# Kernel tuning notes

Measured on AMD Instinct MI355X. Metric: run time of the kernel, lower is better.

Reference implementation:

```python
import jax, jax.numpy as jnp
import numpy as np

B, L, HEADS, D_HEAD = 2, 2048, 16, 64
D_MODEL = HEADS * D_HEAD            # 1024
D_BI = D_MODEL * 4 // 2             # 2048 (bilinear GLU width)
D_PROJ = D_MODEL * 3 + 2 * D_BI
DEPTH = 0                           # block depth < 2 -> token shift active
NEG_INF = -1e10


def _ln(x, g, b, eps=1e-5):
    m = jnp.mean(x, axis=-1, keepdims=True)
    v = jnp.var(x, axis=-1, keepdims=True)
    return (x - m) * jax.lax.rsqrt(v + eps) * g + b


def _shift(x, n):
    # F.pad(x, (0,0,n,-n)): shift along seq dim by n, zero-fill at front
    return jnp.pad(x, ((0, 0), (n, 0), (0, 0)))[:, : x.shape[1], :]


def setup_inputs() -> dict:
    key = jax.random.key(0)
    ks = jax.random.split(key, 3)
    x = jax.random.normal(ks[0], (B, L, D_MODEL), jnp.float32)
    w_in = jax.random.normal(ks[1], (D_MODEL, D_PROJ), jnp.float32) * (D_MODEL ** -0.5)
    # note: torch init zeros out_proj; we use small random weights so backward is non-trivial
    w_out = jax.random.normal(ks[2], (D_MODEL + D_BI, D_MODEL), jnp.float32) * 0.02
    slopes = jnp.concatenate([2.0 ** jnp.linspace(0.0, -6.0, HEADS // 2),
                              jnp.zeros(HEADS - HEADS // 2)]).astype(jnp.float32)
    return {
        "x": x,
        "in_ln_g": jnp.ones(D_MODEL, jnp.float32), "in_ln_b": jnp.zeros(D_MODEL, jnp.float32),
        "mid_ln_g": jnp.ones(D_PROJ, jnp.float32), "mid_ln_b": jnp.zeros(D_PROJ, jnp.float32),
        "out_ln_g": jnp.ones(D_MODEL, jnp.float32), "out_ln_b": jnp.zeros(D_MODEL, jnp.float32),
        "w_in": w_in, "w_out": w_out, "slopes": slopes,
    }


def reference(x, in_ln_g, in_ln_b, mid_ln_g, mid_ln_b, out_ln_g, out_ln_b, w_in, w_out, slopes):
    b, l, d = x.shape
    x = _ln(x, in_ln_g, in_ln_b)
    if DEPTH < 2:
        x = jnp.concatenate([
            _shift(x[..., : d // 4], 1),
            x[..., d // 4: d - d // 8],
            _shift(x[..., d - d // 8:], 2),
        ], axis=-1)
    h = _ln(x @ w_in, mid_ln_g, mid_ln_b)
    q, k, v, p1, p2 = jnp.split(h, [D_MODEL, 2 * D_MODEL, 3 * D_MODEL, 3 * D_MODEL + D_BI], axis=-1)
    to_heads = lambda t: t.reshape(b, l, HEADS, D_HEAD).transpose(0, 2, 1, 3)  # b h l d
    q, k, v = to_heads(q), to_heads(k), to_heads(v)
    logits = jnp.einsum('bhid,bhjd->bhij', q, k) * (D_HEAD ** -0.5)
    pos = jnp.arange(l)
    alibi = pos[None, None, None, :].astype(logits.dtype) * slopes[None, :, None, None]
    causal = jnp.where(pos[:, None] >= pos[None, :], 0.0, NEG_INF).astype(logits.dtype)
    a = jax.nn.softmax(logits + alibi + causal, axis=-1)
    o = jnp.einsum('bhij,bhjd->bhid', a, v).transpose(0, 2, 1, 3).reshape(b, l, d)
    return _ln(jnp.concatenate([o, p1 * p2], axis=-1) @ w_out, out_ln_g, out_ln_b)
```

## Files before the change

### kernel.cpp

```cpp
#include <hip/hip_runtime.h>

#define B_ 2
#define L_ 2048
#define HEADS_ 16
#define DH_ 64
#define DM_ 1024
#define DBI_ 2048
#define DPROJ_ 7168
#define NTOK (B_*L_)
#define DCAT (DM_ + DBI_)

typedef __bf16 bf16;
typedef __attribute__((ext_vector_type(8))) __bf16 bf16x8;
typedef __attribute__((ext_vector_type(4))) float floatx4;

typedef __attribute__((address_space(1))) const void gptr_t;
typedef __attribute__((address_space(3))) void lptr_t;

__device__ __forceinline__ void g2l16(const void* g, void* l) {
    __builtin_amdgcn_global_load_lds((gptr_t*)g, (lptr_t*)l, 16, 0, 0);
}

__global__ __launch_bounds__(256) void transpose_both(const float* __restrict__ w_in,
                                                      const float* __restrict__ w_out,
                                                      bf16* __restrict__ w_inT,
                                                      bf16* __restrict__ w_outT) {
    __shared__ float tile[32][33];
    int l = blockIdx.x;
    const float* in; bf16* outp; int R, C, bx, by;
    if (l < 7168) { in = w_in;  outp = w_inT;  R = DM_;  C = DPROJ_; bx = l % 224; by = l / 224; }
    else { l -= 7168; in = w_out; outp = w_outT; R = DCAT; C = DM_;   bx = l % 32;  by = l / 32; }
    int c0 = bx * 32, r0 = by * 32;
    int x = threadIdx.x & 31, y = threadIdx.x >> 5;
    for (int i = 0; i < 32; i += 8)
        tile[y + i][x] = in[(size_t)(r0 + y + i) * C + (c0 + x)];
    __syncthreads();
    for (int i = 0; i < 32; i += 8)
        outp[(size_t)(c0 + y + i) * R + (r0 + x)] = (bf16)tile[x][y + i];
}

__global__ __launch_bounds__(256) void ln_shift(const float* __restrict__ x,
                                                const float* __restrict__ g,
                                                const float* __restrict__ bb,
                                                bf16* __restrict__ xs) {
    int tok = blockIdx.x;
    int b = tok / L_, l = tok % L_;
    const float* row = x + (size_t)tok * DM_;
    float vals[4];
    float s = 0.f, s2 = 0.f;
    for (int i = 0; i < 4; i++) {
        float v = row[threadIdx.x + i * 256];
        vals[i] = v; s += v; s2 += v * v;
    }
    __shared__ float red[2][4];
    for (int o = 32; o; o >>= 1) { s += __shfl_xor(s, o); s2 += __shfl_xor(s2, o); }
    int w = threadIdx.x >> 6;
    if ((threadIdx.x & 63) == 0) { red[0][w] = s; red[1][w] = s2; }
    __syncthreads();
    s  = red[0][0] + red[0][1] + red[0][2] + red[0][3];
    s2 = red[1][0] + red[1][1] + red[1][2] + red[1][3];
    float mean = s * (1.f / DM_);
    float var  = s2 * (1.f / DM_) - mean * mean;
    float rstd = rsqrtf(var + 1e-5f);
    for (int i = 0; i < 4; i++) {
        int c = threadIdx.x + i * 256;
        float y = (vals[i] - mean) * rstd * g[c] + bb[c];
        int shift = (c < 256) ? 1 : ((c >= 896) ? 2 : 0);
        int dl = l + shift;
        if (dl < L_) xs[((size_t)b * L_ + dl) * DM_ + c] = (bf16)y;
        if (l == 0 && shift) {
            xs[((size_t)b * L_ + 0) * DM_ + c] = (bf16)0.f;
            if (shift == 2) xs[((size_t)b * L_ + 1) * DM_ + c] = (bf16)0.f;
        }
    }
}

__global__ __launch_bounds__(512, 2) void gemm1_fr(const bf16* __restrict__ A,
                                                   const bf16* __restrict__ Bt,
                                                   bf16* __restrict__ C) {
    const int K = DM_, N = DPROJ_;
    int lin = blockIdx.x;
    int xcd = lin & 7, idx = lin >> 3;
    int mt = (xcd >> 2) * 8 + idx / 7;
    int nt = (xcd & 3) * 7 + idx % 7;
    int m0 = mt * 256, n0 = nt * 256;

    __shared__ bf16 As[2][256 * 64];
    __shared__ bf16 Bs[2][256 * 64];

    int t = threadIdx.x;
    int lane = t & 63;
    int c = lane & 15, quad = lane >> 4;
    int wave = t >> 6;
    int wm = (wave >> 2) * 128;
    int wn = (wave & 3) * 64;

    auto stageA = [&](int k0, int bsel, int h) {
        #pragma unroll
        for (int s = 0; s < 2; s++) {
            int g = h * 1024 + s * 512 + t;
            int row = g >> 3;
            int kc = (g & 7) ^ (row & 7);
            g2l16(A + (size_t)(m0 + row) * K + (k0 + kc * 8), &As[bsel][g * 8]);
        }
    };
    auto stageB = [&](int k0, int bsel, int h) {
        #pragma unroll
        for (int s = 0; s < 2; s++) {
            int g = h * 1024 + s * 512 + t;
            int row = g >> 3;
            int kc = (g & 7) ^ (row & 7);
            g2l16(Bt + (size_t)(n0 + row) * K + (k0 + kc * 8), &Bs[bsel][g * 8]);
        }
    };

    floatx4 acc[8][4] = {};

    stageA(0, 0, 0); stageA(0, 0, 1);
    stageB(0, 0, 0); stageB(0, 0, 1);
    stageB(64, 1, 0); stageB(64, 1, 1);
    asm volatile("s_waitcnt vmcnt(4)" ::: "memory");
    __builtin_amdgcn_s_barrier();
    __builtin_amdgcn_sched_barrier(0);

    const int nT = K / 64;
    for (int tt = 0; tt < nT; ++tt) {
        int cur = tt & 1, nxt = cur ^ 1;
        int k1 = (tt + 1) << 6, k2 = (tt + 2) << 6;
        bool dA = (tt + 1 < nT), dB = (tt + 2 < nT);
        bf16x8 bfr[4][2];
        #pragma unroll
        for (int p = 0; p < 4; p++) {
            if      (p == 0) { if (dA) stageA(k1, nxt, 0); }
            else if (p == 1) { if (dA) stageA(k1, nxt, 1); }
            else if (p == 2) { if (dB) stageB(k2, cur, 0); }
            else             { if (dB) stageB(k2, cur, 1); }
            if (p == 0) {
                #pragma unroll
                for (int j = 0; j < 4; j++)
                    #pragma unroll
                    for (int s = 0; s < 2; s++)
                        bfr[j][s] = *(const bf16x8*)&Bs[cur][(wn + j * 16 + c) * 64
                                                            + (((s * 4 + quad) ^ (c & 7)) * 8)];
            }
            bf16x8 af[2][2];
            #pragma unroll
            for (int ii = 0; ii < 2; ii++)
                #pragma unroll
                for (int s = 0; s < 2; s++)
                    af[ii][s] = *(const bf16x8*)&As[cur][(wm + (p * 2 + ii) * 16 + c) * 64
                                                         + (((s * 4 + quad) ^ (c & 7)) * 8)];
            __builtin_amdgcn_s_setprio(1);
            #pragma unroll
            for (int ii = 0; ii < 2; ii++)
                #pragma unroll
                for (int j = 0; j < 4; j++)
                    #pragma unroll
                    for (int s = 0; s < 2; s++)
                        acc[p * 2 + ii][j] = __builtin_amdgcn_mfma_f32_16x16x32_bf16(
                            af[ii][s], bfr[j][s], acc[p * 2 + ii][j], 0, 0, 0);
            __builtin_amdgcn_s_setprio(0);
        }
        asm volatile("s_waitcnt lgkmcnt(0)" ::: "memory");
        if (dB)      { asm volatile("s_waitcnt vmcnt(4)" ::: "memory"); }
        else if (dA) { asm volatile("s_waitcnt vmcnt(0)" ::: "memory"); }
        if (tt + 1 < nT) __builtin_amdgcn_s_barrier();
        __builtin_amdgcn_sched_barrier(0);
    }

    #pragma unroll
    for (int i = 0; i < 8; i++)
        #pragma unroll
        for (int j = 0; j < 4; j++)
            #pragma unroll
            for (int r = 0; r < 4; r++) {
                int row = m0 + wm + i * 16 + quad * 4 + r;
                int col = n0 + wn + j * 16 + c;
                C[(size_t)row * N + col] = (bf16)acc[i][j][r];
            }
}

__global__ __launch_bounds__(256) void gemm2_sk(const bf16* __restrict__ A,
                                                const bf16* __restrict__ Bt,
                                                float* __restrict__ P) {
    const int ldA = DCAT, N = DM_;
    int m0 = blockIdx.x * 128, n0 = blockIdx.y * 128, kz = blockIdx.z;
    const bf16* Ak = A + kz * 1024;
    const bf16* Btk = Bt + kz * 1024;
    float* C = P + (size_t)kz * NTOK * DM_;
    __shared__ bf16 As[2][128 * 32];
    __shared__ bf16 Bs[2][128 * 32];
    int t = threadIdx.x, lane = t & 63, wave = t >> 6;
    int c = lane & 15, quad = lane >> 4;
    int wm = (wave >> 1) * 64, wn = (wave & 1) * 64;
    auto stage = [&](int k0, int bsel) {
        #pragma unroll
        for (int s = 0; s < 2; s++) {
            int f = s * 256 + t;
            int row = f >> 2, kp = (f & 3) * 8;
            g2l16(Ak + (size_t)(m0 + row) * ldA + k0 + kp, &As[bsel][f * 8]);
            g2l16(Btk + (size_t)(n0 + row) * ldA + k0 + kp, &Bs[bsel][f * 8]);
        }
    };
    floatx4 acc[4][4] = {};
    stage(0, 0);
    int buf = 0;
    for (int k0 = 0; k0 < 1024; k0 += 32) {
        __syncthreads();
        if (k0 + 32 < 1024) stage(k0 + 32, buf ^ 1);
        bf16x8 af[4], bfr[4];
        #pragma unroll
        for (int i = 0; i < 4; i++)
            af[i] = *(const bf16x8*)&As[buf][(wm + i * 16 + c) * 32 + quad * 8];
        #pragma unroll
        for (int j = 0; j < 4; j++)
            bfr[j] = *(const bf16x8*)&Bs[buf][(wn + j * 16 + c) * 32 + quad * 8];
        #pragma unroll
        for (int i = 0; i < 4; i++)
            #pragma unroll
            for (int j = 0; j < 4; j++)
                acc[i][j] = __builtin_amdgcn_mfma_f32_16x16x32_bf16(af[i], bfr[j], acc[i][j], 0, 0, 0);
        buf ^= 1;
    }
    #pragma unroll
    for (int i = 0; i < 4; i++)
        #pragma unroll
        for (int j = 0; j < 4; j++)
            #pragma unroll
            for (int r = 0; r < 4; r++) {
                int row = m0 + wm + i * 16 + quad * 4 + r;
                int col = n0 + wn + j * 16 + c;
                C[(size_t)row * N + col] = acc[i][j][r];
            }
}

__global__ __launch_bounds__(256) void mid_ln_fused(const bf16* __restrict__ h,
                                                    const float* __restrict__ g,
                                                    const float* __restrict__ bb,
                                                    bf16* __restrict__ Qp,
                                                    bf16* __restrict__ Kp,
                                                    bf16* __restrict__ Vn,
                                                    bf16* __restrict__ A2) {
    int tok = blockIdx.x;
    int b = tok >> 11, l = tok & 2047;
    size_t base = (size_t)tok * DPROJ_;
    int t = threadIdx.x;
    float v[28];
    float s = 0.f, s2 = 0.f;
    for (int i = 0; i < 28; i++) {
        v[i] = (float)h[base + t + i * 256];
        s += v[i]; s2 += v[i] * v[i];
    }
    __shared__ float red[2][4];
    for (int o = 32; o; o >>= 1) { s += __shfl_xor(s, o); s2 += __shfl_xor(s2, o); }
    int w = t >> 6;
    if ((t & 63) == 0) { red[0][w] = s; red[1][w] = s2; }
    __syncthreads();
    s  = red[0][0] + red[0][1] + red[0][2] + red[0][3];
    s2 = red[1][0] + red[1][1] + red[1][2] + red[1][3];
    float mean = s * (1.f / DPROJ_);
    float var  = s2 * (1.f / DPROJ_) - mean * mean;
    float rstd = rsqrtf(var + 1e-5f);
    #pragma unroll
    for (int i = 0; i < 28; i++) {
        int c = t + i * 256;
        v[i] = (v[i] - mean) * rstd * g[c] + bb[c];
    }
    #pragma unroll
    for (int i = 0; i < 12; i++) {
        int c = t + i * 256;
        int sec = c >> 10;
        int cc = c & 1023;
        int hh = cc >> 6, d = cc & 63;
        size_t idx = (((size_t)b * HEADS_ + hh) * L_ + l) * DH_ + d;
        bf16* dst = (sec == 0) ? Qp : (sec == 1) ? Kp : Vn;
        dst[idx] = (bf16)v[i];
    }
    #pragma unroll
    for (int i = 12; i < 20; i++) {
        int c = t + i * 256;
        A2[(size_t)tok * DCAT + DM_ + (c - 3 * DM_)] = (bf16)(v[i] * v[i + 8]);
    }
}

__global__ __launch_bounds__(256) void vt_pack(const bf16* __restrict__ Vn,
                                               bf16* __restrict__ Vt) {
    __shared__ bf16 tile[32][33];
    int bh = blockIdx.z;
    const bf16* in = Vn + (size_t)bh * L_ * DH_;
    bf16* out = Vt + (size_t)bh * DH_ * L_;
    int l0 = blockIdx.x * 32, d0 = blockIdx.y * 32;
    int x = threadIdx.x & 31, y = threadIdx.x >> 5;
    for (int i = 0; i < 32; i += 8)
        tile[y + i][x] = in[(size_t)(l0 + y + i) * DH_ + d0 + x];
    __syncthreads();
    for (int i = 0; i < 32; i += 8)
        out[(size_t)(d0 + y + i) * L_ + l0 + x] = tile[x][y + i];
}

__global__ __launch_bounds__(256, 4) void attn6(const bf16* __restrict__ Qp,
                                                const bf16* __restrict__ Kp,
                                                const bf16* __restrict__ Vt,
                                                const float* __restrict__ slopes,
                                                bf16* __restrict__ A2) {
    int hd = blockIdx.y, b = blockIdx.z;
    int lin = blockIdx.x + 32 * blockIdx.y + 512 * blockIdx.z;
    int xr = blockIdx.x;
    int qt = ((lin >> 8) & 1) ? (31 - xr) : xr;
    int q0 = qt * 64;
    int t = threadIdx.x, lane = t & 63, wave = t >> 6;
    int quad = lane >> 4, c = lane & 15;
    __shared__ bf16 Ks[2][64 * 64];
    __shared__ bf16 Vs[64 * 64];
    __shared__ bf16 Ps[4][16 * 72];
    int bh = b * HEADS_ + hd;
    const bf16* Qb = Qp + (size_t)bh * L_ * DH_;
    const bf16* Kb = Kp + (size_t)bh * L_ * DH_;
    const bf16* Vb = Vt + (size_t)bh * DH_ * L_;
    const float LOG2E = 1.44269504f;
    float slopeL2 = slopes[hd] * LOG2E;
    const float qscale = 0.125f * LOG2E;

    bf16x8 qf[2];
    int qrow = q0 + wave * 16 + c;
    qf[0] = *(const bf16x8*)(Qb + (size_t)qrow * DH_ + quad * 8);
    qf[1] = *(const bf16x8*)(Qb + (size_t)qrow * DH_ + 32 + quad * 8);
    floatx4 accO[4] = {};
    float lsum[4];
    float mrow[4];
    int i_row0 = q0 + wave * 16 + quad * 4;
    #pragma unroll
    for (int r = 0; r < 4; r++) {
        lsum[r] = 0.f;
        mrow[r] = slopeL2 * (float)(i_row0 + r) + 20.0f;
    }

    int row = t >> 2, kp = (t & 3) * 8;
    auto stageK = [&](int j0, int kb) {
        #pragma unroll
        for (int s = 0; s < 2; s++)
            g2l16(Kb + (size_t)(j0 + row) * DH_ + s * 32 + kp, &Ks[kb][(s * 256 + t) * 8]);
    };
    auto stageV = [&](int j0) {
        #pragma unroll
        for (int s = 0; s < 2; s++)
            g2l16(Vb + (size_t)row * L_ + j0 + s * 32 + kp, &Vs[(s * 256 + t) * 8]);
    };

    bf16* pw = &Ps[wave][0];
    bf16* pwr = pw + (quad * 4) * 72 + c;

    stageK(0, 0);
    asm volatile("s_waitcnt vmcnt(0)" ::: "memory");
    __builtin_amdgcn_s_barrier();
    __builtin_amdgcn_sched_barrier(0);

    int kb = 0;
    for (int j0 = 0; j0 <= q0; j0 += 64) {
        bool dK = (j0 + 64 <= q0);
        stageV(j0);
        if (dK) stageK(j0 + 64, kb ^ 1);

        bool diag = (j0 == q0);
        #pragma unroll
        for (int nt = 0; nt < 4; nt++) {
            floatx4 sacc = {};
            bf16x8 kf0 = *(const bf16x8*)&Ks[kb][(nt * 16 + c) * 32 + quad * 8];
            bf16x8 kf1 = *(const bf16x8*)&Ks[kb][2048 + (nt * 16 + c) * 32 + quad * 8];
            sacc = __builtin_amdgcn_mfma_f32_16x16x32_bf16(qf[0], kf0, sacc, 0, 0, 0);
            sacc = __builtin_amdgcn_mfma_f32_16x16x32_bf16(qf[1], kf1, sacc, 0, 0, 0);
            int j = j0 + nt * 16 + c;
            float aj = slopeL2 * (float)j;
            #pragma unroll
            for (int r = 0; r < 4; r++) {
                float p = exp2f(fmaf(sacc[r], qscale, aj) - mrow[r]);
                if (diag) p = (j <= i_row0 + r) ? p : 0.f;
                lsum[r] += p;
                pwr[r * 72 + nt * 16] = (bf16)p;
            }
        }
        bf16x8 pf0 = *(const bf16x8*)&pw[c * 72 + quad * 8];
        bf16x8 pf1 = *(const bf16x8*)&pw[c * 72 + 32 + quad * 8];

        if (dK) { asm volatile("s_waitcnt vmcnt(2)" ::: "memory"); }
        else    { asm volatile("s_waitcnt vmcnt(0)" ::: "memory"); }
        __builtin_amdgcn_s_barrier();
        __builtin_amdgcn_sched_barrier(0);

        #pragma unroll
        for (int nt = 0; nt < 4; nt++) {
            bf16x8 vf0 = *(const bf16x8*)&Vs[(nt * 16 + c) * 32 + quad * 8];
            bf16x8 vf1 = *(const bf16x8*)&Vs[2048 + (nt * 16 + c) * 32 + quad * 8];
            accO[nt] = __builtin_amdgcn_mfma_f32_16x16x32_bf16(pf0, vf0, accO[nt], 0, 0, 0);
            accO[nt] = __builtin_amdgcn_mfma_f32_16x16x32_bf16(pf1, vf1, accO[nt], 0, 0, 0);
        }
        asm volatile("s_waitcnt lgkmcnt(0)" ::: "memory");
        __builtin_amdgcn_s_barrier();
        __builtin_amdgcn_sched_barrier(0);
        kb ^= 1;
    }
    #pragma unroll
    for (int r = 0; r < 4; r++) {
        float l = lsum[r];
        l += __shfl_xor(l, 1);
        l += __shfl_xor(l, 2);
        l += __shfl_xor(l, 4);
        l += __shfl_xor(l, 8);
        lsum[r] = 1.f / l;
    }
    #pragma unroll
    for (int r = 0; r < 4; r++) {
        size_t orow = (size_t)b * L_ + q0 + wave * 16 + quad * 4 + r;
        #pragma unroll
        for (int nt = 0; nt < 4; nt++)
            A2[orow * DCAT + hd * DH_ + nt * 16 + c] = (bf16)(accO[nt][r] * lsum[r]);
    }
}

__global__ __launch_bounds__(256) void out_ln3(const float* __restrict__ P,
                                               const float* __restrict__ g,
                                               const float* __restrict__ bb,
                                               float* __restrict__ out) {
    size_t base = (size_t)blockIdx.x * DM_;
    const size_t stride = (size_t)NTOK * DM_;
    float v[4];
    float s = 0.f, s2 = 0.f;
    for (int i = 0; i < 4; i++) {
        size_t idx = base + threadIdx.x + i * 256;
        v[i] = P[idx] + P[idx + stride] + P[idx + 2 * stride];
        s += v[i]; s2 += v[i] * v[i];
    }
    __shared__ float red[2][4];
    for (int o = 32; o; o >>= 1) { s += __shfl_xor(s, o); s2 += __shfl_xor(s2, o); }
    int w = threadIdx.x >> 6;
    if ((threadIdx.x & 63) == 0) { red[0][w] = s; red[1][w] = s2; }
    __syncthreads();
    s  = red[0][0] + red[0][1] + red[0][2] + red[0][3];
    s2 = red[1][0] + red[1][1] + red[1][2] + red[1][3];
    float mean = s * (1.f / DM_);
    float var  = s2 * (1.f / DM_) - mean * mean;
    float rstd = rsqrtf(var + 1e-5f);
    for (int i = 0; i < 4; i++) {
        int c = threadIdx.x + i * 256;
        out[base + c] = (v[i] - mean) * rstd * g[c] + bb[c];
    }
}

extern "C" void kernel_launch(void* const* d_in, const int* in_sizes, int n_in,
                              void* d_out, int out_size, void* d_ws, size_t ws_size,
                              hipStream_t stream) {
    const float* x     = (const float*)d_in[0];
    const float* in_g  = (const float*)d_in[1];
    const float* in_b  = (const float*)d_in[2];
    const float* mid_g = (const float*)d_in[3];
    const float* mid_b = (const float*)d_in[4];
    const float* out_g = (const float*)d_in[5];
    const float* out_b = (const float*)d_in[6];
    const float* w_in  = (const float*)d_in[7];
    const float* w_out = (const float*)d_in[8];
    const float* slopes = (const float*)d_in[9];
    float* out = (float*)d_out;

    char* ws = (char*)d_ws;
    size_t off = 0;
    auto alloc = [&](size_t n) { char* p = ws + off; off += (n + 255) & ~(size_t)255; return p; };
    bf16* w_inT  = (bf16*)alloc((size_t)DPROJ_ * DM_ * 2);
    bf16* w_outT = (bf16*)alloc((size_t)DM_ * DCAT * 2);
    bf16* xs     = (bf16*)alloc((size_t)NTOK * DM_ * 2);
    bf16* h      = (bf16*)alloc((size_t)NTOK * DPROJ_ * 2);
    bf16* A2     = (bf16*)alloc((size_t)NTOK * DCAT * 2);
    bf16* Qp     = (bf16*)alloc((size_t)NTOK * DM_ * 2);
    bf16* Kp     = (bf16*)alloc((size_t)NTOK * DM_ * 2);
    bf16* Vn     = (bf16*)alloc((size_t)NTOK * DM_ * 2);
    bf16* Vt = xs;
    float* P = (float*)h;

    hipLaunchKernelGGL(transpose_both, dim3(7168 + 3072), dim3(256), 0, stream,
                       w_in, w_out, w_inT, w_outT);
    hipLaunchKernelGGL(ln_shift, dim3(NTOK), dim3(256), 0, stream, x, in_g, in_b, xs);
    hipLaunchKernelGGL(gemm1_fr, dim3(448), dim3(512), 0, stream, xs, w_inT, h);
    hipLaunchKernelGGL(mid_ln_fused, dim3(NTOK), dim3(256), 0, stream, h, mid_g, mid_b,
                       Qp, Kp, Vn, A2);
    hipLaunchKernelGGL(vt_pack, dim3(L_ / 32, DH_ / 32, B_ * HEADS_), dim3(256), 0, stream, Vn, Vt);
    hipLaunchKernelGGL(attn6, dim3(32, HEADS_, B_), dim3(256), 0, stream, Qp, Kp, Vt, slopes, A2);
    hipLaunchKernelGGL(gemm2_sk, dim3(NTOK / 128, DM_ / 128, 3), dim3(256), 0, stream,
                       A2, w_outT, P);
    hipLaunchKernelGGL(out_ln3, dim3(NTOK), dim3(256), 0, stream, P, out_g, out_b, out);
}
```

Baseline: 307.1 us.

## Rework output GEMM into 2-way split-K pipelined kernel and vectorize layernorm kernels

The output projection GEMM moves from a 3-way split-K with a 32-wide K tile to a 2-way split with 64-wide K tiles. It uses XOR-swizzled LDS, staggered A/B prefetch, explicit waitcnt barriers and setprio, copying the schedule of gemm1. The input, mid and output layernorm kernels switch to vectorized 16-byte loads and stores, and the mid-LN block grows to 448 threads with one 8-element chunk pair per thread. The goal is less partial-sum traffic in the final LN and better memory efficiency. The trade-offs are fewer blocks per split and more register and LDS pressure.

```diff
diff --git a/kernel.cpp b/kernel.cpp
--- a/kernel.cpp
+++ b/kernel.cpp
@@ -12,6 +12,7 @@
 
 typedef __bf16 bf16;
 typedef __attribute__((ext_vector_type(8))) __bf16 bf16x8;
+typedef __attribute__((ext_vector_type(4))) __bf16 bf16x4;
 typedef __attribute__((ext_vector_type(4))) float floatx4;
 
 typedef __attribute__((address_space(1))) const void gptr_t;
@@ -45,33 +46,33 @@
                                                 bf16* __restrict__ xs) {
     int tok = blockIdx.x;
     int b = tok / L_, l = tok % L_;
-    const float* row = x + (size_t)tok * DM_;
-    float vals[4];
-    float s = 0.f, s2 = 0.f;
-    for (int i = 0; i < 4; i++) {
-        float v = row[threadIdx.x + i * 256];
-        vals[i] = v; s += v; s2 += v * v;
-    }
+    int t = threadIdx.x;
+    floatx4 v = *(const floatx4*)(x + (size_t)tok * DM_ + t * 4);
+    float s = v[0] + v[1] + v[2] + v[3];
+    float s2 = v[0]*v[0] + v[1]*v[1] + v[2]*v[2] + v[3]*v[3];
     __shared__ float red[2][4];
     for (int o = 32; o; o >>= 1) { s += __shfl_xor(s, o); s2 += __shfl_xor(s2, o); }
-    int w = threadIdx.x >> 6;
-    if ((threadIdx.x & 63) == 0) { red[0][w] = s; red[1][w] = s2; }
+    int w = t >> 6;
+    if ((t & 63) == 0) { red[0][w] = s; red[1][w] = s2; }
     __syncthreads();
     s  = red[0][0] + red[0][1] + red[0][2] + red[0][3];
     s2 = red[1][0] + red[1][1] + red[1][2] + red[1][3];
     float mean = s * (1.f / DM_);
     float var  = s2 * (1.f / DM_) - mean * mean;
     float rstd = rsqrtf(var + 1e-5f);
-    for (int i = 0; i < 4; i++) {
-        int c = threadIdx.x + i * 256;
-        float y = (vals[i] - mean) * rstd * g[c] + bb[c];
-        int shift = (c < 256) ? 1 : ((c >= 896) ? 2 : 0);
-        int dl = l + shift;
-        if (dl < L_) xs[((size_t)b * L_ + dl) * DM_ + c] = (bf16)y;
-        if (l == 0 && shift) {
-            xs[((size_t)b * L_ + 0) * DM_ + c] = (bf16)0.f;
-            if (shift == 2) xs[((size_t)b * L_ + 1) * DM_ + c] = (bf16)0.f;
-        }
+    int c0 = t * 4;
+    floatx4 gg = *(const floatx4*)(g + c0);
+    floatx4 bv = *(const floatx4*)(bb + c0);
+    bf16x4 y;
+    #pragma unroll
+    for (int i = 0; i < 4; i++) y[i] = (bf16)((v[i] - mean) * rstd * gg[i] + bv[i]);
+    int shift = (c0 < 256) ? 1 : ((c0 >= 896) ? 2 : 0);
+    int dl = l + shift;
+    if (dl < L_) *(bf16x4*)(xs + ((size_t)b * L_ + dl) * DM_ + c0) = y;
+    if (l == 0 && shift) {
+        bf16x4 z = {};
+        *(bf16x4*)(xs + ((size_t)b * L_ + 0) * DM_ + c0) = z;
+        if (shift == 2) *(bf16x4*)(xs + ((size_t)b * L_ + 1) * DM_ + c0) = z;
     }
 }
 
@@ -180,61 +181,102 @@
             }
 }
 
-__global__ __launch_bounds__(256) void gemm2_sk(const bf16* __restrict__ A,
-                                                const bf16* __restrict__ Bt,
-                                                float* __restrict__ P) {
+__global__ __launch_bounds__(256, 2) void gemm2_fr(const bf16* __restrict__ A,
+                                                   const bf16* __restrict__ Bt,
+                                                   float* __restrict__ P) {
     const int ldA = DCAT, N = DM_;
     int m0 = blockIdx.x * 128, n0 = blockIdx.y * 128, kz = blockIdx.z;
-    const bf16* Ak = A + kz * 1024;
-    const bf16* Btk = Bt + kz * 1024;
+    const bf16* Ak = A + kz * 1536;
+    const bf16* Btk = Bt + kz * 1536;
     float* C = P + (size_t)kz * NTOK * DM_;
-    __shared__ bf16 As[2][128 * 32];
-    __shared__ bf16 Bs[2][128 * 32];
+    __shared__ bf16 As[2][128 * 64];
+    __shared__ bf16 Bs[2][128 * 64];
     int t = threadIdx.x, lane = t & 63, wave = t >> 6;
     int c = lane & 15, quad = lane >> 4;
     int wm = (wave >> 1) * 64, wn = (wave & 1) * 64;
-    auto stage = [&](int k0, int bsel) {
+
+    auto stageA = [&](int k0, int bsel, int h) {
         #pragma unroll
         for (int s = 0; s < 2; s++) {
-            int f = s * 256 + t;
-            int row = f >> 2, kp = (f & 3) * 8;
-            g2l16(Ak + (size_t)(m0 + row) * ldA + k0 + kp, &As[bsel][f * 8]);
-            g2l16(Btk + (size_t)(n0 + row) * ldA + k0 + kp, &Bs[bsel][f * 8]);
+            int g = h * 512 + s * 256 + t;
+            int row = g >> 3;
+            int kc = (g & 7) ^ (row & 7);
+            g2l16(Ak + (size_t)(m0 + row) * ldA + k0 + kc * 8, &As[bsel][g * 8]);
         }
     };
+    auto stageB = [&](int k0, int bsel, int h) {
+        #pragma unroll
+        for (int s = 0; s < 2; s++) {
+            int g = h * 512 + s * 256 + t;
+            int row = g >> 3;
+            int kc = (g & 7) ^ (row & 7);
+            g2l16(Btk + (size_t)(n0 + row) * ldA + k0 + kc * 8, &Bs[bsel][g * 8]);
+        }
+    };
+
     floatx4 acc[4][4] = {};
-    stage(0, 0);
-    int buf = 0;
-    for (int k0 = 0; k0 < 1024; k0 += 32) {
-        __syncthreads();
-        if (k0 + 32 < 1024) stage(k0 + 32, buf ^ 1);
-        bf16x8 af[4], bfr[4];
-        #pragma unroll
-        for (int i = 0; i < 4; i++)
-            af[i] = *(const bf16x8*)&As[buf][(wm + i * 16 + c) * 32 + quad * 8];
+
+    stageA(0, 0, 0); stageA(0, 0, 1);
+    stageB(0, 0, 0); stageB(0, 0, 1);
+    stageB(64, 1, 0); stageB(64, 1, 1);
+    asm volatile("s_waitcnt vmcnt(4)" ::: "memory");
+    __builtin_amdgcn_s_barrier();
+    __builtin_amdgcn_sched_barrier(0);
+
+    const int nT = 1536 / 64;
+    for (int tt = 0; tt < nT; ++tt) {
+        int cur = tt & 1, nxt = cur ^ 1;
+        int k1 = (tt + 1) << 6, k2 = (tt + 2) << 6;
+        bool dA = (tt + 1 < nT), dB = (tt + 2 < nT);
+        bf16x8 bfr[4][2];
+        #pragma unroll
+        for (int p = 0; p < 4; p++) {
+            if      (p == 0) { if (dA) stageA(k1, nxt, 0); }
+            else if (p == 1) { if (dA) stageA(k1, nxt, 1); }
+            else if (p == 2) { if (dB) stageB(k2, cur, 0); }
+            else             { if (dB) stageB(k2, cur, 1); }
+            if (p == 0) {
+                #pragma unroll
+                for (int j = 0; j < 4; j++)
+                    #pragma unroll
+                    for (int s = 0; s < 2; s++)
+                        bfr[j][s] = *(const bf16x8*)&Bs[cur][(wn + j * 16 + c) * 64
+                                                            + (((s * 4 + quad) ^ (c & 7)) * 8)];
+            }
+            bf16x8 af[2];
+            #pragma unroll
+            for (int s = 0; s < 2; s++)
+                af[s] = *(const bf16x8*)&As[cur][(wm + p * 16 + c) * 64
+                                                 + (((s * 4 + quad) ^ (c & 7)) * 8)];
+            __builtin_amdgcn_s_setprio(1);
+            #pragma unroll
+            for (int j = 0; j < 4; j++)
+                #pragma unroll
+                for (int s = 0; s < 2; s++)
+                    acc[p][j] = __builtin_amdgcn_mfma_f32_16x16x32_bf16(
+                        af[s], bfr[j][s], acc[p][j], 0, 0, 0);
+            __builtin_amdgcn_s_setprio(0);
+        }
+        asm volatile("s_waitcnt lgkmcnt(0)" ::: "memory");
+        if (dB)      { asm volatile("s_waitcnt vmcnt(4)" ::: "memory"); }
+        else if (dA) { asm volatile("s_waitcnt vmcnt(0)" ::: "memory"); }
+        if (tt + 1 < nT) __builtin_amdgcn_s_barrier();
+        __builtin_amdgcn_sched_barrier(0);
+    }
+
+    #pragma unroll
+    for (int p = 0; p < 4; p++)
         #pragma unroll
         for (int j = 0; j < 4; j++)
-            bfr[j] = *(const bf16x8*)&Bs[buf][(wn + j * 16 + c) * 32 + quad * 8];
-        #pragma unroll
-        for (int i = 0; i < 4; i++)
-            #pragma unroll
-            for (int j = 0; j < 4; j++)
-                acc[i][j] = __builtin_amdgcn_mfma_f32_16x16x32_bf16(af[i], bfr[j], acc[i][j], 0, 0, 0);
-        buf ^= 1;
-    }
-    #pragma unroll
-    for (int i = 0; i < 4; i++)
-        #pragma unroll
-        for (int j = 0; j < 4; j++)
             #pragma unroll
             for (int r = 0; r < 4; r++) {
-                int row = m0 + wm + i * 16 + quad * 4 + r;
+                int row = m0 + wm + p * 16 + quad * 4 + r;
                 int col = n0 + wn + j * 16 + c;
-                C[(size_t)row * N + col] = acc[i][j][r];
+                C[(size_t)row * N + col] = acc[p][j][r];
             }
 }
 
-__global__ __launch_bounds__(256) void mid_ln_fused(const bf16* __restrict__ h,
+__global__ __launch_bounds__(448) void mid_ln_fused(const bf16* __restrict__ h,
                                                     const float* __restrict__ g,
                                                     const float* __restrict__ bb,
                                                     bf16* __restrict__ Qp,
@@ -245,41 +287,60 @@
     int b = tok >> 11, l = tok & 2047;
     size_t base = (size_t)tok * DPROJ_;
     int t = threadIdx.x;
-    float v[28];
+    int c0, c1;
+    if (t < 256) { c0 = 384 + t; c1 = 640 + t; }
+    else { int u = t - 256; c0 = 2 * u; c1 = 2 * u + 1; }
+    bf16x8 r0 = *(const bf16x8*)(h + base + c0 * 8);
+    bf16x8 r1 = *(const bf16x8*)(h + base + c1 * 8);
+    float v0[8], v1[8];
     float s = 0.f, s2 = 0.f;
-    for (int i = 0; i < 28; i++) {
-        v[i] = (float)h[base + t + i * 256];
-        s += v[i]; s2 += v[i] * v[i];
-    }
-    __shared__ float red[2][4];
+    #pragma unroll
+    for (int i = 0; i < 8; i++) {
+        v0[i] = (float)r0[i]; v1[i] = (float)r1[i];
+        s += v0[i] + v1[i]; s2 += v0[i] * v0[i] + v1[i] * v1[i];
+    }
+    __shared__ float red[2][7];
     for (int o = 32; o; o >>= 1) { s += __shfl_xor(s, o); s2 += __shfl_xor(s2, o); }
     int w = t >> 6;
     if ((t & 63) == 0) { red[0][w] = s; red[1][w] = s2; }
     __syncthreads();
-    s  = red[0][0] + red[0][1] + red[0][2] + red[0][3];
-    s2 = red[1][0] + red[1][1] + red[1][2] + red[1][3];
+    s = 0.f; s2 = 0.f;
+    #pragma unroll
+    for (int i = 0; i < 7; i++) { s += red[0][i]; s2 += red[1][i]; }
     float mean = s * (1.f / DPROJ_);
     float var  = s2 * (1.f / DPROJ_) - mean * mean;
     float rstd = rsqrtf(var + 1e-5f);
-    #pragma unroll
-    for (int i = 0; i < 28; i++) {
-        int c = t + i * 256;
-        v[i] = (v[i] - mean) * rstd * g[c] + bb[c];
-    }
-    #pragma unroll
-    for (int i = 0; i < 12; i++) {
-        int c = t + i * 256;
-        int sec = c >> 10;
-        int cc = c & 1023;
-        int hh = cc >> 6, d = cc & 63;
-        size_t idx = (((size_t)b * HEADS_ + hh) * L_ + l) * DH_ + d;
-        bf16* dst = (sec == 0) ? Qp : (sec == 1) ? Kp : Vn;
-        dst[idx] = (bf16)v[i];
-    }
-    #pragma unroll
-    for (int i = 12; i < 20; i++) {
-        int c = t + i * 256;
-        A2[(size_t)tok * DCAT + DM_ + (c - 3 * DM_)] = (bf16)(v[i] * v[i + 8]);
+    floatx4 g0a = *(const floatx4*)(g + c0 * 8),  g0b = *(const floatx4*)(g + c0 * 8 + 4);
+    floatx4 b0a = *(const floatx4*)(bb + c0 * 8), b0b = *(const floatx4*)(bb + c0 * 8 + 4);
+    floatx4 g1a = *(const floatx4*)(g + c1 * 8),  g1b = *(const floatx4*)(g + c1 * 8 + 4);
+    floatx4 b1a = *(const floatx4*)(bb + c1 * 8), b1b = *(const floatx4*)(bb + c1 * 8 + 4);
+    float y0[8], y1[8];
+    #pragma unroll
+    for (int i = 0; i < 4; i++) {
+        y0[i]     = (v0[i]     - mean) * rstd * g0a[i] + b0a[i];
+        y0[i + 4] = (v0[i + 4] - mean) * rstd * g0b[i] + b0b[i];
+        y1[i]     = (v1[i]     - mean) * rstd * g1a[i] + b1a[i];
+        y1[i + 4] = (v1[i + 4] - mean) * rstd * g1b[i] + b1b[i];
+    }
+    if (t < 256) {
+        bf16x8 pv;
+        #pragma unroll
+        for (int i = 0; i < 8; i++) pv[i] = (bf16)(y0[i] * y1[i]);
+        *(bf16x8*)(A2 + (size_t)tok * DCAT + DM_ + t * 8) = pv;
+    } else {
+        auto wchunk = [&](int c8, float* y) {
+            int C0 = c8 * 8;
+            int sec = C0 >> 10, cc = C0 & 1023;
+            int hh = cc >> 6, d = cc & 63;
+            size_t idx = (((size_t)b * HEADS_ + hh) * L_ + l) * DH_ + d;
+            bf16* dst = (sec == 0) ? Qp : (sec == 1) ? Kp : Vn;
+            bf16x8 o;
+            #pragma unroll
+            for (int i = 0; i < 8; i++) o[i] = (bf16)y[i];
+            *(bf16x8*)(dst + idx) = o;
+        };
+        wchunk(c0, y0);
+        wchunk(c1, y1);
     }
 }
 
@@ -417,33 +478,37 @@
     }
 }
 
-__global__ __launch_bounds__(256) void out_ln3(const float* __restrict__ P,
+__global__ __launch_bounds__(256) void out_ln2(const float* __restrict__ P,
                                                const float* __restrict__ g,
                                                const float* __restrict__ bb,
                                                float* __restrict__ out) {
     size_t base = (size_t)blockIdx.x * DM_;
     const size_t stride = (size_t)NTOK * DM_;
-    float v[4];
-    float s = 0.f, s2 = 0.f;
-    for (int i = 0; i < 4; i++) {
-        size_t idx = base + threadIdx.x + i * 256;
-        v[i] = P[idx] + P[idx + stride] + P[idx + 2 * stride];
-        s += v[i]; s2 += v[i] * v[i];
-    }
+    int t = threadIdx.x;
+    floatx4 a = *(const floatx4*)(P + base + t * 4);
+    floatx4 b4 = *(const floatx4*)(P + base + stride + t * 4);
+    floatx4 v;
+    #pragma unroll
+    for (int i = 0; i < 4; i++) v[i] = a[i] + b4[i];
+    float s = v[0] + v[1] + v[2] + v[3];
+    float s2 = v[0]*v[0] + v[1]*v[1] + v[2]*v[2] + v[3]*v[3];
     __shared__ float red[2][4];
     for (int o = 32; o; o >>= 1) { s += __shfl_xor(s, o); s2 += __shfl_xor(s2, o); }
-    int w = threadIdx.x >> 6;
-    if ((threadIdx.x & 63) == 0) { red[0][w] = s; red[1][w] = s2; }
+    int w = t >> 6;
+    if ((t & 63) == 0) { red[0][w] = s; red[1][w] = s2; }
     __syncthreads();
     s  = red[0][0] + red[0][1] + red[0][2] + red[0][3];
     s2 = red[1][0] + red[1][1] + red[1][2] + red[1][3];
     float mean = s * (1.f / DM_);
     float var  = s2 * (1.f / DM_) - mean * mean;
     float rstd = rsqrtf(var + 1e-5f);
-    for (int i = 0; i < 4; i++) {
-        int c = threadIdx.x + i * 256;
-        out[base + c] = (v[i] - mean) * rstd * g[c] + bb[c];
-    }
+    int c0 = t * 4;
+    floatx4 gg = *(const floatx4*)(g + c0);
+    floatx4 bv = *(const floatx4*)(bb + c0);
+    floatx4 o;
+    #pragma unroll
+    for (int i = 0; i < 4; i++) o[i] = (v[i] - mean) * rstd * gg[i] + bv[i];
+    *(floatx4*)(out + base + c0) = o;
 }
 
 extern "C" void kernel_launch(void* const* d_in, const int* in_sizes, int n_in,
@@ -479,11 +544,11 @@
                        w_in, w_out, w_inT, w_outT);
     hipLaunchKernelGGL(ln_shift, dim3(NTOK), dim3(256), 0, stream, x, in_g, in_b, xs);
     hipLaunchKernelGGL(gemm1_fr, dim3(448), dim3(512), 0, stream, xs, w_inT, h);
-    hipLaunchKernelGGL(mid_ln_fused, dim3(NTOK), dim3(256), 0, stream, h, mid_g, mid_b,
+    hipLaunchKernelGGL(mid_ln_fused, dim3(NTOK), dim3(448), 0, stream, h, mid_g, mid_b,
                        Qp, Kp, Vn, A2);
     hipLaunchKernelGGL(vt_pack, dim3(L_ / 32, DH_ / 32, B_ * HEADS_), dim3(256), 0, stream, Vn, Vt);
     hipLaunchKernelGGL(attn6, dim3(32, HEADS_, B_), dim3(256), 0, stream, Qp, Kp, Vt, slopes, A2);
-    hipLaunchKernelGGL(gemm2_sk, dim3(NTOK / 128, DM_ / 128, 3), dim3(256), 0, stream,
+    hipLaunchKernelGGL(gemm2_fr, dim3(NTOK / 128, DM_ / 128, 2), dim3(256), 0, stream,
                        A2, w_outT, P);
-    hipLaunchKernelGGL(out_ln3, dim3(NTOK), dim3(256), 0, stream, P, out_g, out_b, out);
-}
+    hipLaunchKernelGGL(out_ln2, dim3(NTOK), dim3(256), 0, stream, P, out_g, out_b, out);
+}
```

Measured after the change: 335.9 us. +9.4%, slower.
